# Performance work log

Measured on AMD Instinct MI355X. Metric: run time of the kernel, lower is better.

## Reference

```python
import jax, jax.numpy as jnp
import numpy as np

N_NODES = 50000
IN, HID, OUT = 128, 128, 47
N_EDGES = 800000


def _glorot(key, shape):
    fan_in, fan_out = shape[1], shape[0]
    lim = np.sqrt(6.0 / (fan_in + fan_out)).astype(np.float32)
    return jax.random.uniform(key, shape, jnp.float32, -lim, lim)


def setup_inputs() -> dict:
    key = jax.random.key(0)
    ks = jax.random.split(key, 12)
    x = jax.random.normal(ks[0], (N_NODES, IN), jnp.float32)
    src = jax.random.randint(ks[1], (N_EDGES,), 0, N_NODES)
    dst = jax.random.randint(ks[2], (N_EDGES,), 0, N_NODES)
    return {
        "x": x, "src": src, "dst": dst,
        "w_self1": _glorot(ks[3], (HID, IN)),  "w_neigh1": _glorot(ks[4], (HID, IN)),  "b1": jnp.zeros((HID,), jnp.float32),
        "w_self2": _glorot(ks[5], (HID, HID)), "w_neigh2": _glorot(ks[6], (HID, HID)), "b2": jnp.zeros((HID,), jnp.float32),
        "w_self3": _glorot(ks[7], (OUT, HID)), "w_neigh3": _glorot(ks[8], (OUT, HID)), "b3": jnp.zeros((OUT,), jnp.float32),
    }


def _sage_conv(h, src, dst, w_self, w_neigh, b):
    # gather src features, mean-reduce per dst node (DGL copy_u + mean)
    msg = h[src]                                                  # [E, d]
    agg = jax.ops.segment_sum(msg, dst, num_segments=N_NODES)    # [N, d]
    deg = jax.ops.segment_sum(jnp.ones((dst.shape[0],), h.dtype), dst, num_segments=N_NODES)
    mean = agg / jnp.maximum(deg, 1.0)[:, None]
    # DGL SAGEConv('mean'): fc_self(h_dst) + fc_neigh(h_neigh); bias on fc_self only
    return h @ w_self.T + b + mean @ w_neigh.T


def reference(x, src, dst,
              w_self1, w_neigh1, b1,
              w_self2, w_neigh2, b2,
              w_self3, w_neigh3, b3):
    h = _sage_conv(x, src, dst, w_self1, w_neigh1, b1)
    h = jax.nn.relu(h)  # dropout is identity in eval mode
    h = _sage_conv(h, src, dst, w_self2, w_neigh2, b2)
    h = jax.nn.relu(h)
    h = _sage_conv(h, src, dst, w_self3, w_neigh3, b3)
    return h
```

## Files before the change

### kernel.cpp

```cpp
#include <hip/hip_runtime.h>

#define N_NODES 50000
#define N_EDGES 800000
#define DIM 128
#define OUTD 47
#define NBK 196
#define EPB 4096
#define NBIN ((N_EDGES + EPB - 1) / EPB)
#define XCVT_NB (N_NODES * DIM / 8 / 256)
#define WCVT_NB (DIM + DIM + 48)

typedef __attribute__((ext_vector_type(8))) short v8s;
typedef __attribute__((ext_vector_type(8))) unsigned short v8u;
typedef __attribute__((ext_vector_type(4))) float v4f;
typedef __attribute__((ext_vector_type(2))) float v2f;

static __device__ __forceinline__ unsigned short f2bf(float f) {
    union { float f; unsigned int u; } v; v.f = f;
    unsigned int x = v.u;
    return (unsigned short)((x + 0x7fffu + ((x >> 16) & 1u)) >> 16);
}
static __device__ __forceinline__ unsigned char f2fp8(float f) {
    unsigned int pk = __builtin_amdgcn_cvt_pk_fp8_f32(f, f, 0, false);
    return (unsigned char)(pk & 0xffu);
}

__global__ __launch_bounds__(256) void k_prep(const float* __restrict__ x,
                                              unsigned short* __restrict__ xb,
                                              unsigned int* __restrict__ x8,
                                              const int* __restrict__ dst,
                                              int* __restrict__ parts,
                                              const float* __restrict__ ws1, const float* __restrict__ wn1,
                                              const float* __restrict__ ws2, const float* __restrict__ wn2,
                                              const float* __restrict__ ws3, const float* __restrict__ wn3,
                                              unsigned short* __restrict__ wb1,
                                              unsigned short* __restrict__ wb2,
                                              unsigned short* __restrict__ wb3) {
    __shared__ int hist[NBK];
    const int bx = blockIdx.x, tid = threadIdx.x;
    if (bx < XCVT_NB) {
        int i = bx * 256 + tid;
        float4 v0 = ((const float4*)x)[i * 2];
        float4 v1 = ((const float4*)x)[i * 2 + 1];
        ushort4 o0, o1;
        o0.x = f2bf(v0.x); o0.y = f2bf(v0.y); o0.z = f2bf(v0.z); o0.w = f2bf(v0.w);
        o1.x = f2bf(v1.x); o1.y = f2bf(v1.y); o1.z = f2bf(v1.z); o1.w = f2bf(v1.w);
        ((ushort4*)xb)[i * 2] = o0;
        ((ushort4*)xb)[i * 2 + 1] = o1;
        unsigned int a = __builtin_amdgcn_cvt_pk_fp8_f32(v0.x, v0.y, 0, false);
        a = __builtin_amdgcn_cvt_pk_fp8_f32(v0.z, v0.w, a, true);
        unsigned int b = __builtin_amdgcn_cvt_pk_fp8_f32(v1.x, v1.y, 0, false);
        b = __builtin_amdgcn_cvt_pk_fp8_f32(v1.z, v1.w, b, true);
        uint2 o; o.x = a; o.y = b;
        ((uint2*)x8)[i] = o;
    } else if (bx < XCVT_NB + NBIN) {
        const int j = bx - XCVT_NB;
        for (int i = tid; i < NBK; i += 256) hist[i] = 0;
        __syncthreads();
        const int e0 = j * EPB;
        const int ecnt = min(EPB, N_EDGES - e0);
        for (int r = tid; r < ecnt; r += 256)
            atomicAdd(&hist[dst[e0 + r] >> 8], 1);
        __syncthreads();
        for (int i = tid; i < NBK; i += 256) parts[j * NBK + i] = hist[i];
    } else {
        int b2 = bx - XCVT_NB - NBIN;
        const float *sw, *nw; unsigned short* ob; int j, J;
        if (b2 < DIM)            { sw = ws1; nw = wn1; ob = wb1; j = b2;            J = DIM; }
        else if (b2 < 2 * DIM)   { sw = ws2; nw = wn2; ob = wb2; j = b2 - DIM;      J = DIM; }
        else                     { sw = ws3; nw = wn3; ob = wb3; j = b2 - 2 * DIM;  J = OUTD; }
        int k = tid;
        float v = 0.f;
        if (j < J) v = (k < DIM) ? sw[j * DIM + k] : nw[j * DIM + (k - DIM)];
        ob[j * 256 + k] = f2bf(v);
    }
}

__global__ __launch_bounds__(256) void k_bin(const int* __restrict__ src,
                                             const int* __restrict__ dst,
                                             const int* __restrict__ parts,
                                             unsigned int* __restrict__ packed) {
    __shared__ int s[256], gb[NBK], cnt[NBK];
    const int t = threadIdx.x;
    const int j = blockIdx.x;
    int ct = 0, cp = 0;
    for (int i = 0; i < NBIN; ++i) {
        int v = (t < NBK) ? parts[i * NBK + t] : 0;
        if (i == j) cp = ct;
        ct += v;
    }
    s[t] = ct;
    __syncthreads();
    for (int off = 1; off < 256; off <<= 1) {
        int u = (t >= off) ? s[t - off] : 0;
        __syncthreads();
        s[t] += u;
        __syncthreads();
    }
    if (t < NBK) { gb[t] = (s[t] - ct) + cp; cnt[t] = 0; }
    __syncthreads();
    const int e0 = j * EPB;
    const int ecnt = min(EPB, N_EDGES - e0);
    for (int r = t; r < ecnt; r += 256) {
        int sv = src[e0 + r], d = dst[e0 + r];
        int b = d >> 8;
        int loc = atomicAdd(&cnt[b], 1);
        packed[gb[b] + loc] = ((unsigned int)sv << 8) | (unsigned int)(d & 255);
    }
}

__global__ __launch_bounds__(256) void k_place(const unsigned int* __restrict__ packed,
                                               const int* __restrict__ parts,
                                               int* __restrict__ row_ptr,
                                               int* __restrict__ src_sorted) {
    __shared__ int s[256], baseL[NBK], totL[NBK];
    __shared__ int hist[256], cur[256];
    const int b = blockIdx.x, t = threadIdx.x;
    int ct = 0;
    for (int i = 0; i < NBIN; ++i)
        ct += (t < NBK) ? parts[i * NBK + t] : 0;
    s[t] = ct;
    hist[t] = 0;
    __syncthreads();
    for (int off = 1; off < 256; off <<= 1) {
        int u = (t >= off) ? s[t - off] : 0;
        __syncthreads();
        s[t] += u;
        __syncthreads();
    }
    if (t < NBK) { baseL[t] = s[t] - ct; totL[t] = ct; }
    __syncthreads();
    const int base = baseL[b], cb = totL[b];
    for (int i = t; i < cb; i += 256)
        atomicAdd(&hist[packed[base + i] & 255u], 1);
    __syncthreads();
    int v = hist[t];
    s[t] = v;
    __syncthreads();
    for (int off = 1; off < 256; off <<= 1) {
        int u = (t >= off) ? s[t - off] : 0;
        __syncthreads();
        s[t] += u;
        __syncthreads();
    }
    int excl = base + s[t] - v;
    int node = b * 256 + t;
    if (node < N_NODES) row_ptr[node] = excl;
    if (b == NBK - 1 && t == 255) row_ptr[N_NODES] = base + cb;
    cur[t] = excl;
    __syncthreads();
    for (int i = t; i < cb; i += 256) {
        unsigned int pkt = packed[base + i];
        int pos = atomicAdd(&cur[pkt & 255u], 1);
        src_sorted[pos] = (int)(pkt >> 8);
    }
}

__global__ __launch_bounds__(256) void k_agg8(const unsigned char* __restrict__ h8,
                                              const int* __restrict__ row_ptr,
                                              const int* __restrict__ srcs,
                                              unsigned short* __restrict__ meanb) {
    const int tid = threadIdx.x;
    const int lane = tid & 63, wv = tid >> 6;
    const int g = lane & 15, ns = lane >> 4;
    const int n = blockIdx.x * 16 + wv * 4 + ns;
    const int start = row_ptr[n], end = row_ptr[n + 1];
    float a0=0.f,a1=0.f,a2=0.f,a3=0.f,a4=0.f,a5=0.f,a6=0.f,a7=0.f;
    int e = start;
    for (; e + 4 <= end; e += 4) {
        int s0 = srcs[e], s1 = srcs[e + 1], s2 = srcs[e + 2], s3 = srcs[e + 3];
        uint2 u0 = *(const uint2*)(h8 + (size_t)s0 * DIM + g * 8);
        uint2 u1 = *(const uint2*)(h8 + (size_t)s1 * DIM + g * 8);
        uint2 u2 = *(const uint2*)(h8 + (size_t)s2 * DIM + g * 8);
        uint2 u3 = *(const uint2*)(h8 + (size_t)s3 * DIM + g * 8);
        v2f p0 = __builtin_amdgcn_cvt_pk_f32_fp8(u0.x, false);
        v2f p1 = __builtin_amdgcn_cvt_pk_f32_fp8(u0.x, true);
        v2f p2 = __builtin_amdgcn_cvt_pk_f32_fp8(u0.y, false);
        v2f p3 = __builtin_amdgcn_cvt_pk_f32_fp8(u0.y, true);
        v2f q0 = __builtin_amdgcn_cvt_pk_f32_fp8(u1.x, false);
        v2f q1 = __builtin_amdgcn_cvt_pk_f32_fp8(u1.x, true);
        v2f q2 = __builtin_amdgcn_cvt_pk_f32_fp8(u1.y, false);
        v2f q3 = __builtin_amdgcn_cvt_pk_f32_fp8(u1.y, true);
        v2f r0 = __builtin_amdgcn_cvt_pk_f32_fp8(u2.x, false);
        v2f r1 = __builtin_amdgcn_cvt_pk_f32_fp8(u2.x, true);
        v2f r2 = __builtin_amdgcn_cvt_pk_f32_fp8(u2.y, false);
        v2f r3 = __builtin_amdgcn_cvt_pk_f32_fp8(u2.y, true);
        v2f w0 = __builtin_amdgcn_cvt_pk_f32_fp8(u3.x, false);
        v2f w1 = __builtin_amdgcn_cvt_pk_f32_fp8(u3.x, true);
        v2f w2 = __builtin_amdgcn_cvt_pk_f32_fp8(u3.y, false);
        v2f w3 = __builtin_amdgcn_cvt_pk_f32_fp8(u3.y, true);
        a0 += (p0[0] + q0[0]) + (r0[0] + w0[0]);
        a1 += (p0[1] + q0[1]) + (r0[1] + w0[1]);
        a2 += (p1[0] + q1[0]) + (r1[0] + w1[0]);
        a3 += (p1[1] + q1[1]) + (r1[1] + w1[1]);
        a4 += (p2[0] + q2[0]) + (r2[0] + w2[0]);
        a5 += (p2[1] + q2[1]) + (r2[1] + w2[1]);
        a6 += (p3[0] + q3[0]) + (r3[0] + w3[0]);
        a7 += (p3[1] + q3[1]) + (r3[1] + w3[1]);
    }
    for (; e < end; ++e) {
        int s0 = srcs[e];
        uint2 u0 = *(const uint2*)(h8 + (size_t)s0 * DIM + g * 8);
        v2f p0 = __builtin_amdgcn_cvt_pk_f32_fp8(u0.x, false);
        v2f p1 = __builtin_amdgcn_cvt_pk_f32_fp8(u0.x, true);
        v2f p2 = __builtin_amdgcn_cvt_pk_f32_fp8(u0.y, false);
        v2f p3 = __builtin_amdgcn_cvt_pk_f32_fp8(u0.y, true);
        a0 += p0[0]; a1 += p0[1]; a2 += p1[0]; a3 += p1[1];
        a4 += p2[0]; a5 += p2[1]; a6 += p3[0]; a7 += p3[1];
    }
    int d = end - start;
    float inv = (d > 0) ? 1.f / (float)d : 0.f;
    v8u o;
    o[0]=f2bf(a0*inv); o[1]=f2bf(a1*inv); o[2]=f2bf(a2*inv); o[3]=f2bf(a3*inv);
    o[4]=f2bf(a4*inv); o[5]=f2bf(a5*inv); o[6]=f2bf(a6*inv); o[7]=f2bf(a7*inv);
    *(v8u*)(meanb + (size_t)n * DIM + g * 8) = o;
}

template <int JT, int TPW, bool RELU, bool OUTBF>
__global__ __launch_bounds__(256) void k_gemm_lds(const unsigned short* __restrict__ Ab,
                                                  const unsigned short* __restrict__ Mb,
                                                  const unsigned short* __restrict__ Wb,
                                                  const float* __restrict__ bias,
                                                  void* __restrict__ out,
                                                  unsigned char* __restrict__ out8,
                                                  int outdim) {
    __shared__ unsigned short Alds[64 * 256];
    __shared__ unsigned short Wlds[JT * 256];
    const int tid = threadIdx.x;
    const int m0 = blockIdx.x * 64;
    const int j0 = blockIdx.y * JT;
    v8u ar[8];
    #pragma unroll
    for (int i = 0; i < 8; ++i) {
        int t = tid + 256 * i;
        int row = t >> 5, ch = t & 31;
        int node = m0 + row; if (node >= N_NODES) node = N_NODES - 1;
        const unsigned short* s = (ch < 16) ? (Ab + (size_t)node * DIM + ch * 8)
                                            : (Mb + (size_t)node * DIM + (ch - 16) * 8);
        ar[i] = *(const v8u*)s;
    }
    constexpr int WI = (JT * 32 + 255) / 256;
    v8u wr[WI];
    #pragma unroll
    for (int i = 0; i < WI; ++i) {
        int t = tid + 256 * i;
        if (t < JT * 32) {
            int row = t >> 5, ch = t & 31;
            wr[i] = *(const v8u*)(Wb + (size_t)(j0 + row) * 256 + ch * 8);
        }
    }
    #pragma unroll
    for (int i = 0; i < 8; ++i) {
        int t = tid + 256 * i;
        int row = t >> 5, ch = t & 31;
        *(v8u*)(Alds + row * 256 + ((ch * 8) ^ ((row & 7) * 8))) = ar[i];
    }
    #pragma unroll
    for (int i = 0; i < WI; ++i) {
        int t = tid + 256 * i;
        if (t < JT * 32) {
            int row = t >> 5, ch = t & 31;
            *(v8u*)(Wlds + row * 256 + ((ch * 8) ^ ((row & 7) * 8))) = wr[i];
        }
    }
    __syncthreads();
    const int lane = tid & 63, wv = tid >> 6;
    const int m = lane & 15, qd = lane >> 4;
    const int arow = wv * 16 + m;
    v4f acc[TPW] = {};
    #pragma unroll
    for (int c = 0; c < 8; ++c) {
        const int koff = c * 32 + qd * 8;
        v8s af = *(const v8s*)(Alds + arow * 256 + (koff ^ ((arow & 7) * 8)));
        #pragma unroll
        for (int t = 0; t < TPW; ++t) {
            int wrow = t * 16 + m;
            v8s wf = *(const v8s*)(Wlds + wrow * 256 + (koff ^ ((wrow & 7) * 8)));
            acc[t] = __builtin_amdgcn_mfma_f32_16x16x32_bf16(af, wf, acc[t], 0, 0, 0);
        }
    }
    #pragma unroll
    for (int t = 0; t < TPW; ++t) {
        int col = j0 + t * 16 + m;
        bool colok = (col < outdim);
        float bv = colok ? bias[col] : 0.f;
        #pragma unroll
        for (int r = 0; r < 4; ++r) {
            int nrow = m0 + wv * 16 + qd * 4 + r;
            if (colok && nrow < N_NODES) {
                float v = acc[t][r] + bv;
                if (RELU) v = fmaxf(v, 0.f);
                size_t idx = (size_t)nrow * outdim + col;
                if (OUTBF) {
                    ((unsigned short*)out)[idx] = f2bf(v);
                    out8[idx] = f2fp8(v);
                } else {
                    ((float*)out)[idx] = v;
                }
            }
        }
    }
}

extern "C" void kernel_launch(void* const* d_in, const int* in_sizes, int n_in,
                              void* d_out, int out_size, void* d_ws, size_t ws_size,
                              hipStream_t stream) {
    const float* x   = (const float*)d_in[0];
    const int*   src = (const int*)d_in[1];
    const int*   dst = (const int*)d_in[2];
    const float* ws1 = (const float*)d_in[3];
    const float* wn1 = (const float*)d_in[4];
    const float* b1  = (const float*)d_in[5];
    const float* ws2 = (const float*)d_in[6];
    const float* wn2 = (const float*)d_in[7];
    const float* b2  = (const float*)d_in[8];
    const float* ws3 = (const float*)d_in[9];
    const float* wn3 = (const float*)d_in[10];
    const float* b3  = (const float*)d_in[11];

    char* p = (char*)d_ws;
    auto alloc = [&](size_t bytes) { char* r = p; p += (bytes + 255) & ~(size_t)255; return r; };
    int*   row_ptr = (int*)alloc((size_t)(N_NODES + 1) * 4);
    int*   srcs    = (int*)alloc((size_t)N_EDGES * 4);
    unsigned int* packed = (unsigned int*)alloc((size_t)N_EDGES * 4);
    int*   parts   = (int*)alloc((size_t)NBIN * NBK * 4);
    unsigned short* xb    = (unsigned short*)alloc((size_t)N_NODES * DIM * 2);
    unsigned short* meanb = (unsigned short*)alloc((size_t)N_NODES * DIM * 2);
    unsigned short* h1b   = (unsigned short*)alloc((size_t)N_NODES * DIM * 2);
    unsigned short* h2b   = (unsigned short*)alloc((size_t)N_NODES * DIM * 2);
    unsigned char*  h8    = (unsigned char*)alloc((size_t)N_NODES * DIM);
    unsigned short* wb1 = (unsigned short*)alloc((size_t)DIM * 256 * 2);
    unsigned short* wb2 = (unsigned short*)alloc((size_t)DIM * 256 * 2);
    unsigned short* wb3 = (unsigned short*)alloc((size_t)48 * 256 * 2);

    k_prep<<<XCVT_NB + NBIN + WCVT_NB, 256, 0, stream>>>(
        x, xb, (unsigned int*)h8, dst, parts,
        ws1, wn1, ws2, wn2, ws3, wn3, wb1, wb2, wb3);
    k_bin<<<NBIN, 256, 0, stream>>>(src, dst, parts, packed);
    k_place<<<NBK, 256, 0, stream>>>(packed, parts, row_ptr, srcs);

    const int MB = (N_NODES + 63) / 64;
    const int AB = N_NODES / 16;

    k_agg8<<<AB, 256, 0, stream>>>(h8, row_ptr, srcs, meanb);
    k_gemm_lds<64, 4, true, true><<<dim3(MB, 2), 256, 0, stream>>>(xb, meanb, wb1, b1, h1b, h8, DIM);
    k_agg8<<<AB, 256, 0, stream>>>(h8, row_ptr, srcs, meanb);
    k_gemm_lds<64, 4, true, true><<<dim3(MB, 2), 256, 0, stream>>>(h1b, meanb, wb2, b2, h2b, h8, DIM);
    k_agg8<<<AB, 256, 0, stream>>>(h8, row_ptr, srcs, meanb);
    k_gemm_lds<48, 3, false, false><<<dim3(MB, 1), 256, 0, stream>>>(h2b, meanb, wb3, b3, d_out, nullptr, OUTD);
}
```

Before: 261.1 us.

## Switch feature storage and MFMA from bf16/fp8 to fp16 throughout

Replaces the bf16 GEMM operands plus fp8 gather copy with a single fp16 feature buffer used by both aggregation and the f16 MFMA GEMM. Aggregation now gathers fp16 rows and accumulates with packed half-precision vector adds instead of fp8-to-fp32 conversions. This drops the extra fp8 output stores and the conversion ALU work, but doubles bytes gathered per edge and accumulates in fp16, risking precision and overflow issues.

```diff
diff --git a/kernel.cpp b/kernel.cpp
--- a/kernel.cpp
+++ b/kernel.cpp
@@ -10,24 +10,16 @@
 #define XCVT_NB (N_NODES * DIM / 8 / 256)
 #define WCVT_NB (DIM + DIM + 48)
 
-typedef __attribute__((ext_vector_type(8))) short v8s;
+typedef __attribute__((ext_vector_type(8))) _Float16 v8h;
 typedef __attribute__((ext_vector_type(8))) unsigned short v8u;
 typedef __attribute__((ext_vector_type(4))) float v4f;
-typedef __attribute__((ext_vector_type(2))) float v2f;
-
-static __device__ __forceinline__ unsigned short f2bf(float f) {
-    union { float f; unsigned int u; } v; v.f = f;
-    unsigned int x = v.u;
-    return (unsigned short)((x + 0x7fffu + ((x >> 16) & 1u)) >> 16);
-}
-static __device__ __forceinline__ unsigned char f2fp8(float f) {
-    unsigned int pk = __builtin_amdgcn_cvt_pk_fp8_f32(f, f, 0, false);
-    return (unsigned char)(pk & 0xffu);
+
+static __device__ __forceinline__ unsigned short f2h(float f) {
+    union { _Float16 h; unsigned short u; } v; v.h = (_Float16)f; return v.u;
 }
 
 __global__ __launch_bounds__(256) void k_prep(const float* __restrict__ x,
-                                              unsigned short* __restrict__ xb,
-                                              unsigned int* __restrict__ x8,
+                                              unsigned short* __restrict__ x16,
                                               const int* __restrict__ dst,
                                               int* __restrict__ parts,
                                               const float* __restrict__ ws1, const float* __restrict__ wn1,
@@ -42,17 +34,10 @@
         int i = bx * 256 + tid;
         float4 v0 = ((const float4*)x)[i * 2];
         float4 v1 = ((const float4*)x)[i * 2 + 1];
-        ushort4 o0, o1;
-        o0.x = f2bf(v0.x); o0.y = f2bf(v0.y); o0.z = f2bf(v0.z); o0.w = f2bf(v0.w);
-        o1.x = f2bf(v1.x); o1.y = f2bf(v1.y); o1.z = f2bf(v1.z); o1.w = f2bf(v1.w);
-        ((ushort4*)xb)[i * 2] = o0;
-        ((ushort4*)xb)[i * 2 + 1] = o1;
-        unsigned int a = __builtin_amdgcn_cvt_pk_fp8_f32(v0.x, v0.y, 0, false);
-        a = __builtin_amdgcn_cvt_pk_fp8_f32(v0.z, v0.w, a, true);
-        unsigned int b = __builtin_amdgcn_cvt_pk_fp8_f32(v1.x, v1.y, 0, false);
-        b = __builtin_amdgcn_cvt_pk_fp8_f32(v1.z, v1.w, b, true);
-        uint2 o; o.x = a; o.y = b;
-        ((uint2*)x8)[i] = o;
+        v8u o;
+        o[0] = f2h(v0.x); o[1] = f2h(v0.y); o[2] = f2h(v0.z); o[3] = f2h(v0.w);
+        o[4] = f2h(v1.x); o[5] = f2h(v1.y); o[6] = f2h(v1.z); o[7] = f2h(v1.w);
+        *(v8u*)(x16 + (size_t)i * 8) = o;
     } else if (bx < XCVT_NB + NBIN) {
         const int j = bx - XCVT_NB;
         for (int i = tid; i < NBK; i += 256) hist[i] = 0;
@@ -72,7 +57,7 @@
         int k = tid;
         float v = 0.f;
         if (j < J) v = (k < DIM) ? sw[j * DIM + k] : nw[j * DIM + (k - DIM)];
-        ob[j * 256 + k] = f2bf(v);
+        ob[j * 256 + k] = f2h(v);
     }
 }
 
@@ -156,73 +141,45 @@
     }
 }
 
-__global__ __launch_bounds__(256) void k_agg8(const unsigned char* __restrict__ h8,
-                                              const int* __restrict__ row_ptr,
-                                              const int* __restrict__ srcs,
-                                              unsigned short* __restrict__ meanb) {
+__global__ __launch_bounds__(256) void k_agg16(const unsigned short* __restrict__ h16,
+                                               const int* __restrict__ row_ptr,
+                                               const int* __restrict__ srcs,
+                                               unsigned short* __restrict__ meanb) {
     const int tid = threadIdx.x;
     const int lane = tid & 63, wv = tid >> 6;
     const int g = lane & 15, ns = lane >> 4;
     const int n = blockIdx.x * 16 + wv * 4 + ns;
     const int start = row_ptr[n], end = row_ptr[n + 1];
-    float a0=0.f,a1=0.f,a2=0.f,a3=0.f,a4=0.f,a5=0.f,a6=0.f,a7=0.f;
+    v8h accA = {}, accB = {};
     int e = start;
     for (; e + 4 <= end; e += 4) {
         int s0 = srcs[e], s1 = srcs[e + 1], s2 = srcs[e + 2], s3 = srcs[e + 3];
-        uint2 u0 = *(const uint2*)(h8 + (size_t)s0 * DIM + g * 8);
-        uint2 u1 = *(const uint2*)(h8 + (size_t)s1 * DIM + g * 8);
-        uint2 u2 = *(const uint2*)(h8 + (size_t)s2 * DIM + g * 8);
-        uint2 u3 = *(const uint2*)(h8 + (size_t)s3 * DIM + g * 8);
-        v2f p0 = __builtin_amdgcn_cvt_pk_f32_fp8(u0.x, false);
-        v2f p1 = __builtin_amdgcn_cvt_pk_f32_fp8(u0.x, true);
-        v2f p2 = __builtin_amdgcn_cvt_pk_f32_fp8(u0.y, false);
-        v2f p3 = __builtin_amdgcn_cvt_pk_f32_fp8(u0.y, true);
-        v2f q0 = __builtin_amdgcn_cvt_pk_f32_fp8(u1.x, false);
-        v2f q1 = __builtin_amdgcn_cvt_pk_f32_fp8(u1.x, true);
-        v2f q2 = __builtin_amdgcn_cvt_pk_f32_fp8(u1.y, false);
-        v2f q3 = __builtin_amdgcn_cvt_pk_f32_fp8(u1.y, true);
-        v2f r0 = __builtin_amdgcn_cvt_pk_f32_fp8(u2.x, false);
-        v2f r1 = __builtin_amdgcn_cvt_pk_f32_fp8(u2.x, true);
-        v2f r2 = __builtin_amdgcn_cvt_pk_f32_fp8(u2.y, false);
-        v2f r3 = __builtin_amdgcn_cvt_pk_f32_fp8(u2.y, true);
-        v2f w0 = __builtin_amdgcn_cvt_pk_f32_fp8(u3.x, false);
-        v2f w1 = __builtin_amdgcn_cvt_pk_f32_fp8(u3.x, true);
-        v2f w2 = __builtin_amdgcn_cvt_pk_f32_fp8(u3.y, false);
-        v2f w3 = __builtin_amdgcn_cvt_pk_f32_fp8(u3.y, true);
-        a0 += (p0[0] + q0[0]) + (r0[0] + w0[0]);
-        a1 += (p0[1] + q0[1]) + (r0[1] + w0[1]);
-        a2 += (p1[0] + q1[0]) + (r1[0] + w1[0]);
-        a3 += (p1[1] + q1[1]) + (r1[1] + w1[1]);
-        a4 += (p2[0] + q2[0]) + (r2[0] + w2[0]);
-        a5 += (p2[1] + q2[1]) + (r2[1] + w2[1]);
-        a6 += (p3[0] + q3[0]) + (r3[0] + w3[0]);
-        a7 += (p3[1] + q3[1]) + (r3[1] + w3[1]);
+        v8h v0 = *(const v8h*)(h16 + (size_t)s0 * DIM + g * 8);
+        v8h v1 = *(const v8h*)(h16 + (size_t)s1 * DIM + g * 8);
+        v8h v2 = *(const v8h*)(h16 + (size_t)s2 * DIM + g * 8);
+        v8h v3 = *(const v8h*)(h16 + (size_t)s3 * DIM + g * 8);
+        accA += (v0 + v1);
+        accB += (v2 + v3);
     }
     for (; e < end; ++e) {
         int s0 = srcs[e];
-        uint2 u0 = *(const uint2*)(h8 + (size_t)s0 * DIM + g * 8);
-        v2f p0 = __builtin_amdgcn_cvt_pk_f32_fp8(u0.x, false);
-        v2f p1 = __builtin_amdgcn_cvt_pk_f32_fp8(u0.x, true);
-        v2f p2 = __builtin_amdgcn_cvt_pk_f32_fp8(u0.y, false);
-        v2f p3 = __builtin_amdgcn_cvt_pk_f32_fp8(u0.y, true);
-        a0 += p0[0]; a1 += p0[1]; a2 += p1[0]; a3 += p1[1];
-        a4 += p2[0]; a5 += p2[1]; a6 += p3[0]; a7 += p3[1];
-    }
+        accA += *(const v8h*)(h16 + (size_t)s0 * DIM + g * 8);
+    }
+    v8h sum = accA + accB;
     int d = end - start;
     float inv = (d > 0) ? 1.f / (float)d : 0.f;
     v8u o;
-    o[0]=f2bf(a0*inv); o[1]=f2bf(a1*inv); o[2]=f2bf(a2*inv); o[3]=f2bf(a3*inv);
-    o[4]=f2bf(a4*inv); o[5]=f2bf(a5*inv); o[6]=f2bf(a6*inv); o[7]=f2bf(a7*inv);
+    #pragma unroll
+    for (int i = 0; i < 8; ++i) o[i] = f2h((float)sum[i] * inv);
     *(v8u*)(meanb + (size_t)n * DIM + g * 8) = o;
 }
 
-template <int JT, int TPW, bool RELU, bool OUTBF>
+template <int JT, int TPW, bool RELU, bool OUTF16>
 __global__ __launch_bounds__(256) void k_gemm_lds(const unsigned short* __restrict__ Ab,
                                                   const unsigned short* __restrict__ Mb,
                                                   const unsigned short* __restrict__ Wb,
                                                   const float* __restrict__ bias,
                                                   void* __restrict__ out,
-                                                  unsigned char* __restrict__ out8,
                                                   int outdim) {
     __shared__ unsigned short Alds[64 * 256];
     __shared__ unsigned short Wlds[JT * 256];
@@ -271,12 +228,12 @@
     #pragma unroll
     for (int c = 0; c < 8; ++c) {
         const int koff = c * 32 + qd * 8;
-        v8s af = *(const v8s*)(Alds + arow * 256 + (koff ^ ((arow & 7) * 8)));
+        v8h af = *(const v8h*)(Alds + arow * 256 + (koff ^ ((arow & 7) * 8)));
         #pragma unroll
         for (int t = 0; t < TPW; ++t) {
             int wrow = t * 16 + m;
-            v8s wf = *(const v8s*)(Wlds + wrow * 256 + (koff ^ ((wrow & 7) * 8)));
-            acc[t] = __builtin_amdgcn_mfma_f32_16x16x32_bf16(af, wf, acc[t], 0, 0, 0);
+            v8h wf = *(const v8h*)(Wlds + wrow * 256 + (koff ^ ((wrow & 7) * 8)));
+            acc[t] = __builtin_amdgcn_mfma_f32_16x16x32_f16(af, wf, acc[t], 0, 0, 0);
         }
     }
     #pragma unroll
@@ -291,12 +248,8 @@
                 float v = acc[t][r] + bv;
                 if (RELU) v = fmaxf(v, 0.f);
                 size_t idx = (size_t)nrow * outdim + col;
-                if (OUTBF) {
-                    ((unsigned short*)out)[idx] = f2bf(v);
-                    out8[idx] = f2fp8(v);
-                } else {
-                    ((float*)out)[idx] = v;
-                }
+                if (OUTF16) ((unsigned short*)out)[idx] = f2h(v);
+                else        ((float*)out)[idx] = v;
             }
         }
     }
@@ -324,28 +277,26 @@
     int*   srcs    = (int*)alloc((size_t)N_EDGES * 4);
     unsigned int* packed = (unsigned int*)alloc((size_t)N_EDGES * 4);
     int*   parts   = (int*)alloc((size_t)NBIN * NBK * 4);
-    unsigned short* xb    = (unsigned short*)alloc((size_t)N_NODES * DIM * 2);
+    unsigned short* x16   = (unsigned short*)alloc((size_t)N_NODES * DIM * 2);
     unsigned short* meanb = (unsigned short*)alloc((size_t)N_NODES * DIM * 2);
-    unsigned short* h1b   = (unsigned short*)alloc((size_t)N_NODES * DIM * 2);
-    unsigned short* h2b   = (unsigned short*)alloc((size_t)N_NODES * DIM * 2);
-    unsigned char*  h8    = (unsigned char*)alloc((size_t)N_NODES * DIM);
+    unsigned short* h1    = (unsigned short*)alloc((size_t)N_NODES * DIM * 2);
+    unsigned short* h2    = (unsigned short*)alloc((size_t)N_NODES * DIM * 2);
     unsigned short* wb1 = (unsigned short*)alloc((size_t)DIM * 256 * 2);
     unsigned short* wb2 = (unsigned short*)alloc((size_t)DIM * 256 * 2);
     unsigned short* wb3 = (unsigned short*)alloc((size_t)48 * 256 * 2);
 
     k_prep<<<XCVT_NB + NBIN + WCVT_NB, 256, 0, stream>>>(
-        x, xb, (unsigned int*)h8, dst, parts,
-        ws1, wn1, ws2, wn2, ws3, wn3, wb1, wb2, wb3);
+        x, x16, dst, parts, ws1, wn1, ws2, wn2, ws3, wn3, wb1, wb2, wb3);
     k_bin<<<NBIN, 256, 0, stream>>>(src, dst, parts, packed);
     k_place<<<NBK, 256, 0, stream>>>(packed, parts, row_ptr, srcs);
 
     const int MB = (N_NODES + 63) / 64;
     const int AB = N_NODES / 16;
 
-    k_agg8<<<AB, 256, 0, stream>>>(h8, row_ptr, srcs, meanb);
-    k_gemm_lds<64, 4, true, true><<<dim3(MB, 2), 256, 0, stream>>>(xb, meanb, wb1, b1, h1b, h8, DIM);
-    k_agg8<<<AB, 256, 0, stream>>>(h8, row_ptr, srcs, meanb);
-    k_gemm_lds<64, 4, true, true><<<dim3(MB, 2), 256, 0, stream>>>(h1b, meanb, wb2, b2, h2b, h8, DIM);
-    k_agg8<<<AB, 256, 0, stream>>>(h8, row_ptr, srcs, meanb);
-    k_gemm_lds<48, 3, false, false><<<dim3(MB, 1), 256, 0, stream>>>(h2b, meanb, wb3, b3, d_out, nullptr, OUTD);
-}
+    k_agg16<<<AB, 256, 0, stream>>>(x16, row_ptr, srcs, meanb);
+    k_gemm_lds<64, 4, true, true><<<dim3(MB, 2), 256, 0, stream>>>(x16, meanb, wb1, b1, h1, DIM);
+    k_agg16<<<AB, 256, 0, stream>>>(h1, row_ptr, srcs, meanb);
+    k_gemm_lds<64, 4, true, true><<<dim3(MB, 2), 256, 0, stream>>>(h1, meanb, wb2, b2, h2, DIM);
+    k_agg16<<<AB, 256, 0, stream>>>(h2, row_ptr, srcs, meanb);
+    k_gemm_lds<48, 3, false, false><<<dim3(MB, 1), 256, 0, stream>>>(h2, meanb, wb3, b3, d_out, OUTD);
+}
```

After: 280.5 us. +7.5%, slower.
